# Kernel optimization log

Hardware: AMD Instinct MI355X
Metric: run time of the kernel (lower is better)

Reference implementation:

```python
import jax, jax.numpy as jnp
import numpy as np

O, I, K = 64, 64, 3          # out_channels, in_channels, kernel_size
NH, M = 64, 32               # controller hidden, memory slots
TEMP = 0.5                   # base_temp (temp buffer at init)
F_GAMMA = 0.3
DIL = 1
RF = (K - 1) * DIL + 1
PAD = RF // 2                # = 1; RF odd -> remove = 0
B, T = 64, 8192


def setup_inputs() -> dict:
    key = jax.random.key(0)
    ks = jax.random.split(key, 20)
    d = O * I * K              # 12288
    qd = O * (K + 2)           # 320
    Wm = jax.random.normal(ks[3], (qd, M), jnp.float32)
    Wm = Wm / jnp.linalg.norm(Wm, axis=0, keepdims=True)  # column-normalized memory bank
    s = 0.05
    return {
        "x": jax.random.normal(ks[0], (B, I, T), jnp.float32),
        "grads": jax.random.normal(ks[1], (d,), jnp.float32) * 0.01,
        "q_ema": jax.random.normal(ks[2], (qd,), jnp.float32) * 0.01,
        "W": Wm,
        "conv_w": jax.random.normal(ks[4], (O, I, K), jnp.float32) * s,
        "conv_b": jax.random.normal(ks[5], (O,), jnp.float32) * s,
        "ctrl_w": jax.random.normal(ks[6], (NH, I * K), jnp.float32) * s,
        "ctrl_b": jax.random.normal(ks[7], (NH,), jnp.float32) * s,
        "cw_w": jax.random.normal(ks[8], (K, NH), jnp.float32) * s,
        "cw_b": jax.random.normal(ks[9], (K,), jnp.float32) * s,
        "cb_w": jax.random.normal(ks[10], (1, NH), jnp.float32) * s,
        "cb_b": jax.random.normal(ks[11], (1,), jnp.float32) * s,
        "cf_w": jax.random.normal(ks[12], (1, NH), jnp.float32) * s,
        "cf_b": jax.random.normal(ks[13], (1,), jnp.float32) * s,
        "tau_w1": jax.random.normal(ks[14], (16, NH), jnp.float32) * s,
        "tau_b1": jax.random.normal(ks[15], (16,), jnp.float32) * s,
        "tau_w2": jax.random.normal(ks[16], (1, 16), jnp.float32) * s,
        "tau_b2": jax.random.normal(ks[17], (1,), jnp.float32) * s,
        "trigger": 1,
    }


def reference(x, grads, q_ema, W, conv_w, conv_b, ctrl_w, ctrl_b, cw_w, cw_b,
              cb_w, cb_b, cf_w, cf_b, tau_w1, tau_b1, tau_w2, tau_b2, trigger):
    # --- fw_chunks: per-out-channel controller MLP (dropout is eval-mode identity) ---
    g = grads.reshape(O, I * K)                               # [O, I*K]
    rep = jax.nn.silu(g @ ctrl_w.T + ctrl_b)                  # [O, NH]
    w = rep @ cw_w.T + cw_b                                   # [O, K]
    b = (rep @ cb_w.T + cb_b)[:, 0]                           # [O]
    f = (rep @ cf_w.T + cf_b)[:, 0]                           # [O]
    tau = jnp.mean(jax.nn.sigmoid(
        jax.nn.silu(rep @ tau_w1.T + tau_b1) @ tau_w2.T + tau_b2)) * 0.5 + 0.5

    q = jnp.concatenate([w.reshape(-1), b, f])                # [O*(K+2)]
    # q_ema in-place EMA update happens BEFORE the 0.5/0.5 blend in torch
    q_ema_new = F_GAMMA * q_ema + (1.0 - F_GAMMA) * jax.lax.stop_gradient(q)
    q = 0.5 * q + 0.5 * q_ema_new

    if trigger == 1:  # memory-bank topk attention retrieval
        q_det = jax.lax.stop_gradient(q)
        att = jax.nn.softmax((q_det @ W) / TEMP)              # [M]
        v, idx = jax.lax.top_k(att, 3)
        old_q = (W[:, idx] * v).sum(axis=1)                   # [q_dim]
        q = tau * q + (1.0 - tau) * jax.lax.stop_gradient(old_q)

    ws = O * K
    wq = q[:ws].reshape(O, K)[:, None, :]                     # [O,1,K]
    bq = q[ws:ws + O]                                         # [O]
    fq = q[ws + O:]                                           # [O]

    # --- modulated conv1d ---
    cw = conv_w * wq                                          # [O,I,K]
    out = jax.lax.conv_general_dilated(
        x, cw, window_strides=(1,), padding=[(PAD, PAD)],
        rhs_dilation=(DIL,), dimension_numbers=("NCH", "OIH", "NCH"))
    out = out + (conv_b * bq)[None, :, None]
    out = fq[None, :, None] * out                             # [B,O,T]; remove=0 (RF odd)
    return out
```

## Files before the change

kernel.cpp:

```cpp
#include <hip/hip_runtime.h>
#include <math.h>

#define TT 128
#define TP 72

typedef short bf16x8 __attribute__((ext_vector_type(8)));
typedef float f32x4 __attribute__((ext_vector_type(4)));
typedef unsigned short u16x8 __attribute__((ext_vector_type(8)));

__device__ __forceinline__ unsigned short f2bf(float f) {
  union { float f; unsigned int u; } v; v.f = f;
  unsigned int u = v.u;
  u += 0x7fffu + ((u >> 16) & 1u);
  return (unsigned short)(u >> 16);
}

__global__ void k_rep(const float* __restrict__ grads, const float* __restrict__ ctrl_w,
                      const float* __restrict__ ctrl_b, float* __restrict__ rep_out) {
  int idx = blockIdx.x * 256 + threadIdx.x;
  int r = idx >> 6, c = idx & 63;
  const float4* g4 = (const float4*)(grads + r * 192);
  const float4* w4 = (const float4*)(ctrl_w + c * 192);
  float acc = ctrl_b[c];
  #pragma unroll 8
  for (int j = 0; j < 48; ++j) {
    float4 a = g4[j], b = w4[j];
    acc += a.x * b.x + a.y * b.y + a.z * b.z + a.w * b.w;
  }
  float sg = 1.0f / (1.0f + expf(-acc));
  rep_out[idx] = acc * sg;
}

__global__ void k_qpipe(const float* __restrict__ rep, const float* __restrict__ q_ema,
    const float* __restrict__ W, const float* __restrict__ conv_w, const float* __restrict__ conv_b,
    const float* __restrict__ cw_w, const float* __restrict__ cw_b,
    const float* __restrict__ cb_w, const float* __restrict__ cb_b,
    const float* __restrict__ cf_w, const float* __restrict__ cf_b,
    const float* __restrict__ tau_w1, const float* __restrict__ tau_b1,
    const float* __restrict__ tau_w2, const float* __restrict__ tau_b2,
    const int* __restrict__ trigger,
    unsigned short* __restrict__ scw, float* __restrict__ sbias) {
  __shared__ float s_q1[320];
  __shared__ float s_q2[320];
  __shared__ float s_h[64 * 17];
  __shared__ float s_s[64];
  __shared__ float s_part[320];
  __shared__ float s_att[32];
  __shared__ float s_red[4];
  __shared__ int   s_idx[3];
  int tid = threadIdx.x;

  {
    const float* wrow; float bias; int r;
    if (tid < 192)      { r = tid / 3; int k = tid - r * 3; wrow = cw_w + k * 64; bias = cw_b[k]; }
    else if (tid < 256) { r = tid - 192; wrow = cb_w; bias = cb_b[0]; }
    else                { r = tid - 256; wrow = cf_w; bias = cf_b[0]; }
    float acc = bias;
    const float4* rp = (const float4*)(rep + r * 64);
    const float4* wp = (const float4*)wrow;
    #pragma unroll
    for (int j = 0; j < 16; ++j) {
      float4 a = rp[j], b = wp[j];
      acc += a.x * b.x + a.y * b.y + a.z * b.z + a.w * b.w;
    }
    s_q1[tid] = 0.85f * acc + 0.15f * q_ema[tid];
  }
  for (int e = tid; e < 1024; e += 320) {
    int r = e >> 4, u = e & 15;
    float acc = tau_b1[u];
    const float4* rp = (const float4*)(rep + r * 64);
    const float4* wp = (const float4*)(tau_w1 + u * 64);
    #pragma unroll
    for (int j = 0; j < 16; ++j) {
      float4 a = rp[j], b = wp[j];
      acc += a.x * b.x + a.y * b.y + a.z * b.z + a.w * b.w;
    }
    s_h[r * 17 + u] = acc / (1.0f + expf(-acc));
  }
  __syncthreads();
  if (tid < 64) {
    float acc = tau_b2[0];
    #pragma unroll
    for (int u = 0; u < 16; ++u) acc += s_h[tid * 17 + u] * tau_w2[u];
    s_s[tid] = 1.0f / (1.0f + expf(-acc));
  }
  {
    int m = tid & 31, pg = tid >> 5;
    float acc = 0.f;
    #pragma unroll
    for (int pp = 0; pp < 32; ++pp) {
      int p = pg * 32 + pp;
      acc += s_q1[p] * W[p * 32 + m];
    }
    s_part[tid] = acc;
  }
  __syncthreads();
  if (tid < 32) {
    float acc = 0.f;
    #pragma unroll
    for (int pg = 0; pg < 10; ++pg) acc += s_part[pg * 32 + tid];
    s_att[tid] = acc * 2.0f;
  }
  __syncthreads();
  if (tid == 0) {
    float tau = 0.f;
    for (int r = 0; r < 64; ++r) tau += s_s[r];
    tau = tau * (1.0f / 64.0f) * 0.5f + 0.5f;
    float mx = s_att[0];
    for (int m = 1; m < 32; ++m) mx = fmaxf(mx, s_att[m]);
    float pr[32]; float sum = 0.f;
    #pragma unroll
    for (int m = 0; m < 32; ++m) { pr[m] = expf(s_att[m] - mx); sum += pr[m]; }
    float inv = 1.0f / sum;
    int i0 = -1, i1 = -1, i2 = -1; float v0 = -1.f, v1 = -1.f, v2 = -1.f;
    #pragma unroll
    for (int m = 0; m < 32; ++m) {
      float v = pr[m];
      if (v > v0)      { v2 = v1; i2 = i1; v1 = v0; i1 = i0; v0 = v; i0 = m; }
      else if (v > v1) { v2 = v1; i2 = i1; v1 = v; i1 = m; }
      else if (v > v2) { v2 = v; i2 = m; }
    }
    s_red[0] = tau; s_red[1] = v0 * inv; s_red[2] = v1 * inv; s_red[3] = v2 * inv;
    s_idx[0] = i0; s_idx[1] = i1; s_idx[2] = i2;
  }
  __syncthreads();
  {
    float q1 = s_q1[tid];
    float q2;
    if (trigger[0] == 1) {
      float tau = s_red[0];
      float oq = W[tid * 32 + s_idx[0]] * s_red[1]
               + W[tid * 32 + s_idx[1]] * s_red[2]
               + W[tid * 32 + s_idx[2]] * s_red[3];
      q2 = tau * q1 + (1.0f - tau) * oq;
    } else {
      q2 = q1;
    }
    s_q2[tid] = q2;
  }
  __syncthreads();
  for (int e = tid; e < 12288; e += 320) {
    int k = e >> 12, rem = e & 4095;
    int o = rem >> 6, i = rem & 63;
    float val = conv_w[(o * 64 + i) * 3 + k] * s_q2[o * 3 + k] * s_q2[256 + o];
    scw[e] = f2bf(val);
  }
  if (tid < 64) sbias[tid] = s_q2[256 + tid] * conv_b[tid] * s_q2[192 + tid];
}

__global__ __launch_bounds__(256, 4) void k_conv(const float* __restrict__ x,
    const unsigned short* __restrict__ scw, const float* __restrict__ sbias,
    float* __restrict__ out) {
  __shared__ __align__(16) unsigned short xs[130 * TP];
  __shared__ float sb[64];
  const int tid = threadIdx.x;
  const int b = blockIdx.y;
  const int t0 = blockIdx.x * TT;

  const int lane = tid & 63;
  const int wv   = tid >> 6;
  const int quad = lane >> 4;
  const int l15  = lane & 15;
  const int wt   = (wv & 1) * 64;
  const int wo   = (wv >> 1) * 32;

  if (tid < 64) sb[tid] = sbias[tid];

  bf16x8 wfr[3][2][2];
  #pragma unroll
  for (int k = 0; k < 3; ++k)
    #pragma unroll
    for (int ii = 0; ii < 2; ++ii)
      #pragma unroll
      for (int n = 0; n < 2; ++n)
        wfr[k][ii][n] = *(const bf16x8*)(scw + k * 4096 + (wo + n * 16 + l15) * 64 + ii * 32 + quad * 8);

  const int q   = tid & 31;
  const int oct = tid >> 5;
  const float* xb = x + (size_t)b * (64 * 8192);
  const float* xp = xb + (size_t)(oct * 8) * 8192 + t0 + q * 4;
  f32x4 arr[8];
  #pragma unroll
  for (int rr = 0; rr < 8; ++rr)
    arr[rr] = *(const f32x4*)(xp + (size_t)rr * 8192);

  float hv = 0.0f;
  if (tid < 128) {
    const int side = tid >> 6;
    const int i    = tid & 63;
    const int tg   = side ? (t0 + TT) : (t0 - 1);
    if (tg >= 0 && tg < 8192) hv = xb[(size_t)i * 8192 + tg];
  }

  #pragma unroll
  for (int e = 0; e < 4; ++e) {
    u16x8 v;
    #pragma unroll
    for (int rr = 0; rr < 8; ++rr) v[rr] = f2bf(arr[rr][e]);
    *(u16x8*)(xs + (q * 4 + e + 1) * TP + oct * 8) = v;
  }
  if (tid < 128) {
    const int side = tid >> 6;
    const int i    = tid & 63;
    xs[(side ? 129 : 0) * TP + i] = f2bf(hv);
  }

  __syncthreads();

  f32x4 acc[4][2];
  #pragma unroll
  for (int m = 0; m < 4; ++m)
    #pragma unroll
    for (int n = 0; n < 2; ++n)
      acc[m][n] = (f32x4){0.f, 0.f, 0.f, 0.f};

  const char* xsb = (const char*)xs + (wt + l15) * (TP * 2) + quad * 16;
  #pragma unroll
  for (int k = 0; k < 3; ++k) {
    #pragma unroll
    for (int ii = 0; ii < 2; ++ii) {
      #pragma unroll
      for (int m = 0; m < 4; ++m) {
        const bf16x8 afr = *(const bf16x8*)(xsb + (m * 16 + k) * (TP * 2) + ii * 64);
        acc[m][0] = __builtin_amdgcn_mfma_f32_16x16x32_bf16(afr, wfr[k][ii][0], acc[m][0], 0, 0, 0);
        acc[m][1] = __builtin_amdgcn_mfma_f32_16x16x32_bf16(afr, wfr[k][ii][1], acc[m][1], 0, 0, 0);
      }
    }
  }

  #pragma unroll
  for (int m = 0; m < 4; ++m) {
    #pragma unroll
    for (int n = 0; n < 2; ++n) {
      const int o = wo + n * 16 + l15;
      const float bias = sb[o];
      f32x4 v = acc[m][n];
      v[0] += bias; v[1] += bias; v[2] += bias; v[3] += bias;
      float* op = out + ((size_t)(b * 64 + o)) * 8192 + t0 + wt + m * 16 + quad * 4;
      *(f32x4*)op = v;
    }
  }
}

extern "C" void kernel_launch(void* const* d_in, const int* in_sizes, int n_in,
                              void* d_out, int out_size, void* d_ws, size_t ws_size,
                              hipStream_t stream) {
  const float* x      = (const float*)d_in[0];
  const float* grads  = (const float*)d_in[1];
  const float* q_ema  = (const float*)d_in[2];
  const float* W      = (const float*)d_in[3];
  const float* conv_w = (const float*)d_in[4];
  const float* conv_b = (const float*)d_in[5];
  const float* ctrl_w = (const float*)d_in[6];
  const float* ctrl_b = (const float*)d_in[7];
  const float* cw_w   = (const float*)d_in[8];
  const float* cw_b   = (const float*)d_in[9];
  const float* cb_w   = (const float*)d_in[10];
  const float* cb_b   = (const float*)d_in[11];
  const float* cf_w   = (const float*)d_in[12];
  const float* cf_b   = (const float*)d_in[13];
  const float* tau_w1 = (const float*)d_in[14];
  const float* tau_b1 = (const float*)d_in[15];
  const float* tau_w2 = (const float*)d_in[16];
  const float* tau_b2 = (const float*)d_in[17];
  const int*   trigger = (const int*)d_in[18];
  float* out = (float*)d_out;

  float*          ws_rep   = (float*)d_ws;
  unsigned short* ws_scw   = (unsigned short*)((char*)d_ws + 16384);
  float*          ws_sbias = (float*)((char*)d_ws + 16384 + 24576);

  k_rep<<<16, 256, 0, stream>>>(grads, ctrl_w, ctrl_b, ws_rep);
  k_qpipe<<<1, 320, 0, stream>>>(ws_rep, q_ema, W, conv_w, conv_b, cw_w, cw_b, cb_w, cb_b,
                                 cf_w, cf_b, tau_w1, tau_b1, tau_w2, tau_b2, trigger,
                                 ws_scw, ws_sbias);
  k_conv<<<dim3(64, 64), 256, 0, stream>>>(x, ws_scw, ws_sbias, out);
}
```

Measured before the change: 302.9 us.

## Make conv blocks persistent over four time tiles with double-buffered LDS prefetch

Each conv block now handles four consecutive time tiles instead of one, and the grid shrinks to a quarter of its former size. While the MFMAs run on the current LDS buffer, the next tile's x data is prefetched into registers and then written to a second buffer. The aim is to spread the per-block weight-fragment and bias load over more work and to hide global-load latency. The cost is doubled LDS use and fewer blocks, so occupancy may drop and the GPU may be less evenly filled.

```diff
diff --git a/kernel.cpp b/kernel.cpp
--- a/kernel.cpp
+++ b/kernel.cpp
@@ -3,6 +3,7 @@
 
 #define TT 128
 #define TP 72
+#define NT 4
 
 typedef short bf16x8 __attribute__((ext_vector_type(8)));
 typedef float f32x4 __attribute__((ext_vector_type(4)));
@@ -151,11 +152,11 @@
 __global__ __launch_bounds__(256, 4) void k_conv(const float* __restrict__ x,
     const unsigned short* __restrict__ scw, const float* __restrict__ sbias,
     float* __restrict__ out) {
-  __shared__ __align__(16) unsigned short xs[130 * TP];
+  __shared__ __align__(16) unsigned short xs[2][130 * TP];
   __shared__ float sb[64];
   const int tid = threadIdx.x;
   const int b = blockIdx.y;
-  const int t0 = blockIdx.x * TT;
+  const int tile0 = blockIdx.x * NT;
 
   const int lane = tid & 63;
   const int wv   = tid >> 6;
@@ -177,68 +178,83 @@
 
   const int q   = tid & 31;
   const int oct = tid >> 5;
+  const int hside = tid >> 6;
+  const int hi    = tid & 63;
   const float* xb = x + (size_t)b * (64 * 8192);
-  const float* xp = xb + (size_t)(oct * 8) * 8192 + t0 + q * 4;
+
   f32x4 arr[8];
-  #pragma unroll
-  for (int rr = 0; rr < 8; ++rr)
-    arr[rr] = *(const f32x4*)(xp + (size_t)rr * 8192);
-
   float hv = 0.0f;
-  if (tid < 128) {
-    const int side = tid >> 6;
-    const int i    = tid & 63;
-    const int tg   = side ? (t0 + TT) : (t0 - 1);
-    if (tg >= 0 && tg < 8192) hv = xb[(size_t)i * 8192 + tg];
-  }
-
-  #pragma unroll
-  for (int e = 0; e < 4; ++e) {
-    u16x8 v;
-    #pragma unroll
-    for (int rr = 0; rr < 8; ++rr) v[rr] = f2bf(arr[rr][e]);
-    *(u16x8*)(xs + (q * 4 + e + 1) * TP + oct * 8) = v;
-  }
-  if (tid < 128) {
-    const int side = tid >> 6;
-    const int i    = tid & 63;
-    xs[(side ? 129 : 0) * TP + i] = f2bf(hv);
-  }
-
-  __syncthreads();
-
-  f32x4 acc[4][2];
-  #pragma unroll
-  for (int m = 0; m < 4; ++m)
-    #pragma unroll
-    for (int n = 0; n < 2; ++n)
-      acc[m][n] = (f32x4){0.f, 0.f, 0.f, 0.f};
-
-  const char* xsb = (const char*)xs + (wt + l15) * (TP * 2) + quad * 16;
-  #pragma unroll
-  for (int k = 0; k < 3; ++k) {
-    #pragma unroll
-    for (int ii = 0; ii < 2; ++ii) {
-      #pragma unroll
-      for (int m = 0; m < 4; ++m) {
-        const bf16x8 afr = *(const bf16x8*)(xsb + (m * 16 + k) * (TP * 2) + ii * 64);
-        acc[m][0] = __builtin_amdgcn_mfma_f32_16x16x32_bf16(afr, wfr[k][ii][0], acc[m][0], 0, 0, 0);
-        acc[m][1] = __builtin_amdgcn_mfma_f32_16x16x32_bf16(afr, wfr[k][ii][1], acc[m][1], 0, 0, 0);
+
+  auto load_tile = [&](int t0) {
+    const float* xp = xb + (size_t)(oct * 8) * 8192 + t0 + q * 4;
+    #pragma unroll
+    for (int rr = 0; rr < 8; ++rr)
+      arr[rr] = *(const f32x4*)(xp + (size_t)rr * 8192);
+    hv = 0.0f;
+    if (tid < 128) {
+      const int tg = hside ? (t0 + TT) : (t0 - 1);
+      if (tg >= 0 && tg < 8192) hv = xb[(size_t)hi * 8192 + tg];
+    }
+  };
+  auto write_tile = [&](unsigned short* bufp) {
+    #pragma unroll
+    for (int e = 0; e < 4; ++e) {
+      u16x8 v;
+      #pragma unroll
+      for (int rr = 0; rr < 8; ++rr) v[rr] = f2bf(arr[rr][e]);
+      *(u16x8*)(bufp + (q * 4 + e + 1) * TP + oct * 8) = v;
+    }
+    if (tid < 128) bufp[(hside ? 129 : 0) * TP + hi] = f2bf(hv);
+  };
+
+  load_tile(tile0 * TT);
+  write_tile(&xs[0][0]);
+
+  for (int j = 0; j < NT; ++j) {
+    __syncthreads();
+
+    if (j < NT - 1) {
+      load_tile((tile0 + j + 1) * TT);
+      __builtin_amdgcn_sched_barrier(0);
+    }
+
+    const unsigned short* cur = &xs[j & 1][0];
+    f32x4 acc[4][2];
+    #pragma unroll
+    for (int m = 0; m < 4; ++m)
+      #pragma unroll
+      for (int n = 0; n < 2; ++n)
+        acc[m][n] = (f32x4){0.f, 0.f, 0.f, 0.f};
+
+    const char* xsb = (const char*)cur + (wt + l15) * (TP * 2) + quad * 16;
+    #pragma unroll
+    for (int k = 0; k < 3; ++k) {
+      #pragma unroll
+      for (int ii = 0; ii < 2; ++ii) {
+        #pragma unroll
+        for (int m = 0; m < 4; ++m) {
+          const bf16x8 afr = *(const bf16x8*)(xsb + (m * 16 + k) * (TP * 2) + ii * 64);
+          acc[m][0] = __builtin_amdgcn_mfma_f32_16x16x32_bf16(afr, wfr[k][ii][0], acc[m][0], 0, 0, 0);
+          acc[m][1] = __builtin_amdgcn_mfma_f32_16x16x32_bf16(afr, wfr[k][ii][1], acc[m][1], 0, 0, 0);
+        }
       }
     }
-  }
-
-  #pragma unroll
-  for (int m = 0; m < 4; ++m) {
-    #pragma unroll
-    for (int n = 0; n < 2; ++n) {
-      const int o = wo + n * 16 + l15;
-      const float bias = sb[o];
-      f32x4 v = acc[m][n];
-      v[0] += bias; v[1] += bias; v[2] += bias; v[3] += bias;
-      float* op = out + ((size_t)(b * 64 + o)) * 8192 + t0 + wt + m * 16 + quad * 4;
-      *(f32x4*)op = v;
-    }
+
+    const int t0 = (tile0 + j) * TT;
+    #pragma unroll
+    for (int m = 0; m < 4; ++m) {
+      #pragma unroll
+      for (int n = 0; n < 2; ++n) {
+        const int o = wo + n * 16 + l15;
+        const float bias = sb[o];
+        f32x4 v = acc[m][n];
+        v[0] += bias; v[1] += bias; v[2] += bias; v[3] += bias;
+        float* op = out + ((size_t)(b * 64 + o)) * 8192 + t0 + wt + m * 16 + quad * 4;
+        *(f32x4*)op = v;
+      }
+    }
+
+    if (j < NT - 1) write_tile(&xs[(j + 1) & 1][0]);
   }
 }
 
@@ -274,5 +290,5 @@
   k_qpipe<<<1, 320, 0, stream>>>(ws_rep, q_ema, W, conv_w, conv_b, cw_w, cw_b, cb_w, cb_b,
                                  cf_w, cf_b, tau_w1, tau_b1, tau_w2, tau_b2, trigger,
                                  ws_scw, ws_sbias);
-  k_conv<<<dim3(64, 64), 256, 0, stream>>>(x, ws_scw, ws_sbias, out);
-}
+  k_conv<<<dim3(16, 64), 256, 0, stream>>>(x, ws_scw, ws_sbias, out);
+}
```

Result: slower. 330.8 us (+9.2%).
